# Kernel optimization log

Measured on AMD Instinct MI355X. Metric: run time of the kernel, lower is better.

## Reference

```python
import jax, jax.numpy as jnp
import numpy as np
from jax import lax

D = 256      # d_model
NH = 4       # nhead == len(multi_size)
DH = D // NH # per-head dim = 64
B, H, W = 8, 32, 32
EPS_LN = 1e-5
EPS_ATT = 1e-6


def conv2d(x, w, pad):
    # x: [B,C,H,W], w: [O,I,k,k], SAME padding via pad=k//2
    return lax.conv_general_dilated(
        x, w, window_strides=(1, 1), padding=[(pad, pad), (pad, pad)],
        dimension_numbers=("NCHW", "OIHW", "NCHW"))


def layer_norm(x, g, b):
    m = jnp.mean(x, axis=-1, keepdims=True)
    v = jnp.mean((x - m) ** 2, axis=-1, keepdims=True)
    return (x - m) * lax.rsqrt(v + EPS_LN) * g + b


def setup_inputs() -> dict:
    key = jax.random.key(0)
    ks = jax.random.split(key, 20)
    s = 0.02
    inp = {
        "x": jax.random.normal(ks[0], (B, D, H, W), jnp.float32),
        "source": jax.random.normal(ks[1], (B, D, H, W), jnp.float32),
        # q projection: conv3x3 d_model -> d_model (bias-free)
        "Wq": jax.random.normal(ks[2], (D, D, 3, 3), jnp.float32) * s,
        # MultiConv k projection: kernels 1,3,5,7, each d_model -> dim
        "Wk1": jax.random.normal(ks[3], (DH, D, 1, 1), jnp.float32) * s,
        "Wk3": jax.random.normal(ks[4], (DH, D, 3, 3), jnp.float32) * s,
        "Wk5": jax.random.normal(ks[5], (DH, D, 5, 5), jnp.float32) * s,
        "Wk7": jax.random.normal(ks[6], (DH, D, 7, 7), jnp.float32) * s,
        # MultiConv v projection
        "Wv1": jax.random.normal(ks[7], (DH, D, 1, 1), jnp.float32) * s,
        "Wv3": jax.random.normal(ks[8], (DH, D, 3, 3), jnp.float32) * s,
        "Wv5": jax.random.normal(ks[9], (DH, D, 5, 5), jnp.float32) * s,
        "Wv7": jax.random.normal(ks[10], (DH, D, 7, 7), jnp.float32) * s,
        # merge linear (bias=False), stored [in,out]
        "Wm": jax.random.normal(ks[11], (D, D), jnp.float32) * s,
        "ln1_g": jnp.ones((D,), jnp.float32),
        "ln1_b": jnp.zeros((D,), jnp.float32),
        "ln2_g": jnp.ones((D,), jnp.float32),
        "ln2_b": jnp.zeros((D,), jnp.float32),
        # FF mlp: Linear(2D->2D, no bias), ReLU, Linear(2D->D, no bias); [in,out]
        "W1": jax.random.normal(ks[12], (2 * D, 2 * D), jnp.float32) * s,
        "W2": jax.random.normal(ks[13], (2 * D, D), jnp.float32) * s,
    }
    return inp


def _forward(x, source, Wq, Wk1, Wk3, Wk5, Wk7, Wv1, Wv3, Wv5, Wv7,
             Wm, ln1_g, ln1_b, ln2_g, ln2_b, W1, W2):
    b, c, h, w = x.shape
    h1, w1 = source.shape[2], source.shape[3]
    L = h * w
    S = h1 * w1

    # projections (multi-scale convs -> heads along channel)
    q = conv2d(x, Wq, 1)                                        # [b,D,h,w]
    k = jnp.concatenate([conv2d(source, Wk1, 0), conv2d(source, Wk3, 1),
                         conv2d(source, Wk5, 2), conv2d(source, Wk7, 3)], axis=1)
    v = jnp.concatenate([conv2d(source, Wv1, 0), conv2d(source, Wv3, 1),
                         conv2d(source, Wv5, 2), conv2d(source, Wv7, 3)], axis=1)

    # b c h w -> b (h w) (nhead dim) -> b L nhead dim
    q = q.transpose(0, 2, 3, 1).reshape(b, L, NH, DH)
    k = k.transpose(0, 2, 3, 1).reshape(b, S, NH, DH)
    v = v.transpose(0, 2, 3, 1).reshape(b, S, NH, DH)

    # FullAttention_vis: softmax attention map [b, L, S, nhead]
    temp = DH ** -0.5
    qk = jnp.einsum("blhd,bshd->blsh", q, k)
    attn_vis = jax.nn.softmax(qk * temp, axis=2)

    # LinearAttention (elu+1 kernel feature map)
    Qf = jax.nn.elu(q) + 1.0
    Kf = jax.nn.elu(k) + 1.0
    v_len = jnp.float32(S)
    vals = v / v_len
    KV = jnp.einsum("bshd,bshv->bhdv", Kf, vals)                # [b,NH,DH,DH]
    Z = 1.0 / (jnp.einsum("blhd,bhd->blh", Qf, Kf.sum(axis=1)) + EPS_ATT)
    msg = jnp.einsum("blhd,bhdv,blh->blhv", Qf, KV, Z) * v_len  # [b,L,NH,DH]

    # merge + norm1
    msg = layer_norm(msg.reshape(b, L, D) @ Wm, ln1_g, ln1_b)

    # FF (mlp): cat -> Linear -> ReLU -> Linear -> norm2
    xf = x.transpose(0, 2, 3, 1).reshape(b, L, c)
    ff = jax.nn.relu(jnp.concatenate([xf, msg], axis=2) @ W1) @ W2
    msg = layer_norm(ff, ln2_g, ln2_b)                          # [b,L,D]
    msg = msg.reshape(b, h, w, c).transpose(0, 3, 1, 2)         # b c h w

    out = x + msg
    # b (h0 w0) (h1 w1) c -> b c h0 w0 h1 w1
    vis = attn_vis.reshape(b, h, w, h1, w1, NH).transpose(0, 5, 1, 2, 3, 4)
    return out, vis


def reference(x, source, Wq, Wk1, Wk3, Wk5, Wk7, Wv1, Wv3, Wv5, Wv7,
              Wm, ln1_g, ln1_b, ln2_g, ln2_b, W1, W2):
    return _forward(x, source, Wq, Wk1, Wk3, Wk5, Wk7, Wv1, Wv3, Wv5, Wv7,
                    Wm, ln1_g, ln1_b, ln2_g, ln2_b, W1, W2)
```

## Files before the change

### kernel.cpp

```cpp
#include <hip/hip_runtime.h>

#define DEV __device__ __forceinline__

typedef unsigned short u16;
typedef unsigned int u32;
typedef __bf16 bf16x8 __attribute__((ext_vector_type(8)));
typedef float f32x4 __attribute__((ext_vector_type(4)));

DEV float elu1(float x) { return x > 0.f ? x + 1.f : __expf(x); }

DEV u16 f2bf(float f) {
    union { float f; unsigned u; } v; v.f = f;
    unsigned r = v.u + 0x7fffu + ((v.u >> 16) & 1u);
    return (u16)(r >> 16);
}

DEV float bf2f(u16 h) {
    union { u32 u; float f; } v; v.u = ((u32)h) << 16; return v.f;
}

__global__ __launch_bounds__(256) void prep1_kernel(
    const float* __restrict__ Wq,
    const float* __restrict__ Wk1, const float* __restrict__ Wk3,
    const float* __restrict__ Wk5, const float* __restrict__ Wk7,
    const float* __restrict__ Wv1, const float* __restrict__ Wv3,
    const float* __restrict__ Wv5, const float* __restrict__ Wv7,
    u16* __restrict__ wpack,
    const float* __restrict__ x, const float* __restrict__ src,
    u16* __restrict__ xbh, u16* __restrict__ sbh)
{
    __shared__ float lds[32 * 129];
    const int t = threadIdx.x;
    if (blockIdx.x < 1632) {
        int gid = blockIdx.x * 256 + t;
        int frag = gid >> 6, l = gid & 63;
        const float* W; int K, ocbase = 0, rel;
        if (frag < 1152) {
            W = Wq; K = 3; int slot = frag / 288; rel = frag % 288; ocbase = slot * 64;
        } else {
            int f = frag - 1152; int side = f / 2688; f %= 2688;
            if (f < 32)        { W = side ? Wv1 : Wk1; K = 1; rel = f; }
            else if (f < 320)  { W = side ? Wv3 : Wk3; K = 3; rel = f - 32; }
            else if (f < 1120) { W = side ? Wv5 : Wk5; K = 5; rel = f - 320; }
            else               { W = side ? Wv7 : Wk7; K = 7; rel = f - 1120; }
        }
        int og = rel & 3, cc = (rel >> 2) & 7, tap = rel >> 5;
        int dy = tap / K, dx = tap % K;
        int oc = ocbase + og * 16 + (l & 15);
        int c0 = cc * 32 + (l >> 4) * 8;
        u16 pk[8];
#pragma unroll
        for (int j = 0; j < 8; ++j)
            pk[j] = f2bf(W[((size_t)(oc * 256 + c0 + j) * K + dy) * K + dx]);
        *(int4*)&wpack[(size_t)frag * 512 + l * 8] = *(const int4*)pk;
        return;
    }
    const int i = blockIdx.x - 1632;
    const int inp = i >> 9, rem = i & 511;
    const int b = rem >> 6, cc = (rem >> 3) & 7, pxb = rem & 7;
    const float* in = (inp ? src : x) + ((size_t)b * 256 + cc * 32) * 1024 + pxb * 128;
    u16* outp = (inp ? sbh : xbh) + (size_t)b * 262144 + (size_t)cc * 32768 + pxb * 128 * 32;
#pragma unroll
    for (int u = 0; u < 4; ++u) {
        int unit = t + u * 256;
        int r = unit >> 5, px4 = unit & 31;
        float4 v = *(const float4*)(in + (size_t)r * 1024 + px4 * 4);
        lds[r * 129 + px4 * 4 + 0] = v.x;
        lds[r * 129 + px4 * 4 + 1] = v.y;
        lds[r * 129 + px4 * 4 + 2] = v.z;
        lds[r * 129 + px4 * 4 + 3] = v.w;
    }
    __syncthreads();
#pragma unroll
    for (int u = 0; u < 2; ++u) {
        int unit = t + u * 256;
        int px = unit >> 2, cg = unit & 3;
        u16 pk[8];
#pragma unroll
        for (int j = 0; j < 8; ++j) pk[j] = f2bf(lds[(cg * 8 + j) * 129 + px]);
        *(int4*)&outp[px * 32 + cg * 8] = *(const int4*)pk;
    }
}

template<int K>
DEV void conv_mfma_body(const u16* __restrict__ srcb,
                        const u16* __restrict__ wsec,
                        u16* __restrict__ dst,
                        u16* Bt, int y0, int cch0, int ncc, int t)
{
    constexpr int P = K / 2;
    const int w = t >> 6, l = t & 63;
    const int chi = l >> 4, ln = l & 15;
    const int rowbase = chi * 22 + w * 2 + 3 - P;
    const int colbase = ln + 3 - P;
    f32x4 acc[4][4];
#pragma unroll
    for (int m = 0; m < 4; ++m)
#pragma unroll
        for (int n = 0; n < 4; ++n) acc[m][n] = (f32x4){0.f, 0.f, 0.f, 0.f};

    for (int cc = 0; cc < ncc; ++cc) {
        const int ccg = cch0 + cc;
        __syncthreads();
#pragma unroll
        for (int u = 0; u < 7; ++u) {
            int unit = t + (u << 9);
            if (unit < 2816) {
                int xv = unit & 31, r = unit >> 5;
                int yy = r % 22, ch = r / 22;
                int ygl = y0 - 3 + yy;
                int4 pk;
                if ((unsigned)ygl < 32u)
                    pk = *(const int4*)&srcb[(size_t)ccg * 32768 + (ygl * 32 + xv) * 32 + ch * 8];
                else
                    pk = (int4){0, 0, 0, 0};
                *(int4*)&Bt[((ch * 22 + yy) * 40 + xv + 3) * 8] = pk;
            } else if (unit < 3520) {
                int hu = unit - 2816;
                int hx = hu & 7; int xi = hx < 3 ? hx : hx + 32;
                int r = hu >> 3; int yy = r % 22, ch = r / 22;
                int4 z = {0, 0, 0, 0};
                *(int4*)&Bt[((ch * 22 + yy) * 40 + xi) * 8] = z;
            }
        }
        __syncthreads();
#pragma unroll
        for (int dy = 0; dy < K; ++dy) {
#pragma unroll
            for (int dx = 0; dx < K; ++dx) {
                const int tap = dy * K + dx;
                const u16* wp = wsec + ((size_t)(tap * 8 + ccg) * 4) * 512 + l * 8;
                bf16x8 a0 = *(const bf16x8*)(wp);
                bf16x8 a1 = *(const bf16x8*)(wp + 512);
                bf16x8 a2 = *(const bf16x8*)(wp + 1024);
                bf16x8 a3 = *(const bf16x8*)(wp + 1536);
                bf16x8 bf[4];
#pragma unroll
                for (int n = 0; n < 4; ++n) {
                    int row = rowbase + dy + (n >> 1);
                    int col = colbase + dx + (n & 1) * 16;
                    bf[n] = *(const bf16x8*)&Bt[(row * 40 + col) * 8];
                }
#pragma unroll
                for (int n = 0; n < 4; ++n) {
                    acc[0][n] = __builtin_amdgcn_mfma_f32_16x16x32_bf16(a0, bf[n], acc[0][n], 0, 0, 0);
                    acc[1][n] = __builtin_amdgcn_mfma_f32_16x16x32_bf16(a1, bf[n], acc[1][n], 0, 0, 0);
                    acc[2][n] = __builtin_amdgcn_mfma_f32_16x16x32_bf16(a2, bf[n], acc[2][n], 0, 0, 0);
                    acc[3][n] = __builtin_amdgcn_mfma_f32_16x16x32_bf16(a3, bf[n], acc[3][n], 0, 0, 0);
                }
            }
        }
    }
#pragma unroll
    for (int m = 0; m < 4; ++m)
#pragma unroll
        for (int n = 0; n < 4; ++n) {
            int y = y0 + w * 2 + (n >> 1);
            int px = y * 32 + (n & 1) * 16 + ln;
            int ocb = m * 16 + chi * 4;
            u16 pk[4];
#pragma unroll
            for (int r = 0; r < 4; ++r) pk[r] = f2bf(acc[m][n][r]);
            *(uint2*)&dst[(size_t)px * 64 + ocb] = *(const uint2*)pk;
        }
}

__global__ __launch_bounds__(512) void conv_mfma_kernel(
    const u16* __restrict__ xbh, const u16* __restrict__ sbh,
    const u16* __restrict__ wpack,
    u16* __restrict__ qbt, u16* __restrict__ kbt, u16* __restrict__ vbt,
    u16* __restrict__ p5u, u16* __restrict__ p7u)
{
    __shared__ u16 Bt[4 * 22 * 40 * 8];
    const int bx = blockIdx.x, t = threadIdx.x;
    const int g = bx & 31, b = (bx >> 5) & 7, m = bx >> 8;
    if (g < 4) {
        conv_mfma_body<3>(xbh + (size_t)b * 262144,
                          wpack + (size_t)(g * 288) * 512,
                          qbt + ((size_t)(b * 4 + g)) * 65536,
                          Bt, m * 16, 0, 8, t);
        return;
    }
    const int gs = g - 4;
    const int side = gs / 14, gg = gs % 14;
    const u16* sp = sbh + (size_t)b * 262144;
    u16* fin = side ? vbt : kbt;
    const size_t wkb = 1152 + (size_t)side * 2688;
    if (gg == 0) {
        conv_mfma_body<1>(sp, wpack + (wkb + 0) * 512,
                          fin + ((size_t)(b * 4 + 0)) * 65536, Bt, m * 16, 0, 8, t);
    } else if (gg == 1) {
        conv_mfma_body<3>(sp, wpack + (wkb + 32) * 512,
                          fin + ((size_t)(b * 4 + 1)) * 65536, Bt, m * 16, 0, 8, t);
    } else if (gg < 6) {
        int cpart = gg - 2;
        conv_mfma_body<5>(sp, wpack + (wkb + 320) * 512,
                          p5u + (((size_t)side * 4 + cpart) * 8 + b) * 65536,
                          Bt, m * 16, cpart * 2, 2, t);
    } else {
        int cpart = gg - 6;
        conv_mfma_body<7>(sp, wpack + (wkb + 1120) * 512,
                          p7u + (((size_t)side * 8 + cpart) * 8 + b) * 65536,
                          Bt, m * 16, cpart, 1, t);
    }
}

__global__ __launch_bounds__(256) void prep2_kernel(
    const u16* __restrict__ p5u, const u16* __restrict__ p7u,
    u16* __restrict__ kbt, u16* __restrict__ vbt,
    const float* __restrict__ W1, const float* __restrict__ W2,
    const float* __restrict__ Wm,
    u16* __restrict__ w1p, u16* __restrict__ w2p, u16* __restrict__ wmp)
{
    const int t = threadIdx.x;
    if (blockIdx.x < 1024) {
        int gid = blockIdx.x * 256 + t;
        int u8 = gid & 8191;
        int b = (gid >> 13) & 7;
        int headk = (gid >> 16) & 1;
        int side = gid >> 17;
        float sacc[8];
#pragma unroll
        for (int e = 0; e < 8; ++e) sacc[e] = 0.f;
        if (headk == 0) {
#pragma unroll
            for (int p = 0; p < 4; ++p) {
                int4 u = *(const int4*)&p5u[(((size_t)side * 4 + p) * 8 + b) * 65536 + (size_t)u8 * 8];
                const u16* uu = (const u16*)&u;
#pragma unroll
                for (int e = 0; e < 8; ++e) sacc[e] += bf2f(uu[e]);
            }
        } else {
#pragma unroll
            for (int p = 0; p < 8; ++p) {
                int4 u = *(const int4*)&p7u[(((size_t)side * 8 + p) * 8 + b) * 65536 + (size_t)u8 * 8];
                const u16* uu = (const u16*)&u;
#pragma unroll
                for (int e = 0; e < 8; ++e) sacc[e] += bf2f(uu[e]);
            }
        }
        u16 pk[8];
#pragma unroll
        for (int e = 0; e < 8; ++e) pk[e] = f2bf(sacc[e]);
        u16* outb = side ? vbt : kbt;
        *(int4*)&outb[((size_t)(b * 4 + 2 + headk)) * 65536 + (size_t)u8 * 8] = *(const int4*)pk;
        return;
    }
    int gid = (blockIdx.x - 1024) * 256 + t;
    int f = gid >> 6, l = gid & 63;
    if (f >= 896) return;
    u16 pk[8];
    if (f < 512) {
        int ks = f >> 5, nf = f & 31;
#pragma unroll
        for (int j = 0; j < 8; ++j)
            pk[j] = f2bf(W1[(size_t)(ks * 32 + (l >> 4) * 8 + j) * 512 + nf * 16 + (l & 15)]);
        *(int4*)&w1p[(size_t)f * 512 + l * 8] = *(const int4*)pk;
    } else if (f < 768) {
        int f2 = f - 512;
        int ks = f2 >> 4, nf = f2 & 15;
#pragma unroll
        for (int j = 0; j < 8; ++j)
            pk[j] = f2bf(W2[(size_t)(ks * 32 + (l >> 4) * 8 + j) * 256 + nf * 16 + (l & 15)]);
        *(int4*)&w2p[(size_t)f2 * 512 + l * 8] = *(const int4*)pk;
    } else {
        int f3 = f - 768;
        int ks = f3 >> 4, nf = f3 & 15;
#pragma unroll
        for (int j = 0; j < 8; ++j)
            pk[j] = f2bf(Wm[(size_t)(ks * 32 + (l >> 4) * 8 + j) * 256 + nf * 16 + (l & 15)]);
        *(int4*)&wmp[(size_t)f3 * 512 + l * 8] = *(const int4*)pk;
    }
}

__global__ __launch_bounds__(256) void prep3_kernel(
    const u16* __restrict__ kbt, const u16* __restrict__ vbt,
    float* __restrict__ KVp, float* __restrict__ Ksump)
{
    __shared__ float4 smem4[2112];
    float* Kt = (float*)smem4;
    float* Vt = (float*)(smem4 + 64 * 17);
    const int t = threadIdx.x;
    const int bx = blockIdx.x;
    const int b = bx >> 4, h = (bx >> 2) & 3, ch = bx & 3;
    const u16* kbase = kbt + ((size_t)(b * 4 + h) * 1024 + ch * 256) * 64;
    const u16* vbase = vbt + ((size_t)(b * 4 + h) * 1024 + ch * 256) * 64;
    const int d = t >> 2, v0 = (t & 3) * 16;
    float4 acc[4];
#pragma unroll
    for (int j = 0; j < 4; ++j) acc[j] = make_float4(0.f, 0.f, 0.f, 0.f);
    float ks = 0.f;
    for (int st = 0; st < 4; ++st) {
        __syncthreads();
        {
            int s = t >> 2, d0 = (t & 3) * 16;
            const u16* krow = kbase + (size_t)(st * 64 + s) * 64;
            const u16* vrow = vbase + (size_t)(st * 64 + s) * 64;
#pragma unroll
            for (int oo = 0; oo < 2; ++oo) {
                int4 k8 = *(const int4*)&krow[d0 + oo * 8];
                int4 v8 = *(const int4*)&vrow[d0 + oo * 8];
                const u16* ku = (const u16*)&k8;
                const u16* vu = (const u16*)&v8;
#pragma unroll
                for (int e = 0; e < 8; ++e) {
                    Kt[s * 68 + d0 + oo * 8 + e] = elu1(bf2f(ku[e]));
                    Vt[s * 64 + d0 + oo * 8 + e] = bf2f(vu[e]);
                }
            }
        }
        __syncthreads();
#pragma unroll 8
        for (int s = 0; s < 64; ++s) {
            float kf = Kt[s * 68 + d];
            const float4* vvp = (const float4*)(Vt + s * 64 + v0);
#pragma unroll
            for (int j = 0; j < 4; ++j) {
                float4 vv = vvp[j];
                acc[j].x += kf * vv.x; acc[j].y += kf * vv.y;
                acc[j].z += kf * vv.z; acc[j].w += kf * vv.w;
            }
        }
        if (t < 64) {
#pragma unroll 8
            for (int s = 0; s < 64; ++s) ks += Kt[s * 68 + t];
        }
    }
    float* op = KVp + ((size_t)((ch * 32 + b * 4 + h) * 64 + d)) * 64 + v0;
#pragma unroll
    for (int j = 0; j < 4; ++j) ((float4*)op)[j] = acc[j];
    if (t < 64) Ksump[(size_t)(ch * 32 + b * 4 + h) * 64 + t] = ks;
}

__global__ __launch_bounds__(512) void qk_sm_msg_kernel(
    const u16* __restrict__ qbt, const u16* __restrict__ kbt,
    float* __restrict__ vis,
    const float* __restrict__ KVp, const float* __restrict__ Ksump,
    float* __restrict__ msg)
{
    __shared__ float4 smem4[4178];
    const int t = threadIdx.x;
    if (blockIdx.x < 1024) {
        u16* kf = (u16*)smem4;
        u16* qf = (u16*)smem4 + 32 * 512;
        float* redM = (float*)((char*)smem4 + 36864);
        float* redS = redM + 256;
        const int bx = blockIdx.x;
        const int b = bx >> 7, h = (bx >> 5) & 3, l0 = (bx & 31) * 32;
        const u16* qtp = qbt + ((size_t)(b * 4 + h)) * 1024 * 64;
        const u16* ktp = kbt + ((size_t)(b * 4 + h)) * 1024 * 64;

        if (t < 256) {
            int r = t & 31, dblk = t >> 5;
            int4 pk = *(const int4*)&qtp[(size_t)(l0 + r) * 64 + dblk * 8];
            *(int4*)&qf[(((r >> 4) * 2 + (dblk >> 2)) * 64 + (dblk & 3) * 16 + (r & 15)) * 8] = pk;
        }
        __syncthreads();

        const int w = t >> 6, l = t & 63, ln = l & 15, lg = l >> 4;
        bf16x8 a[2][2];
#pragma unroll
        for (int fr = 0; fr < 2; ++fr)
#pragma unroll
            for (int ks = 0; ks < 2; ++ks)
                a[fr][ks] = *(const bf16x8*)&qf[((fr * 2 + ks) * 64 + l) * 8];

        f32x4 acc[2][4][2];
#pragma unroll
        for (int fr = 0; fr < 2; ++fr)
#pragma unroll
            for (int cc = 0; cc < 4; ++cc)
#pragma unroll
                for (int f = 0; f < 2; ++f) acc[fr][cc][f] = (f32x4){0.f, 0.f, 0.f, 0.f};

#pragma unroll
        for (int cc = 0; cc < 4; ++cc) {
            __syncthreads();
#pragma unroll
            for (int it = 0; it < 4; ++it) {
                int unit = it * 512 + t;
                int sl = unit & 255, dblk = unit >> 8;
                int4 pk = *(const int4*)&ktp[(size_t)(cc * 256 + sl) * 64 + dblk * 8];
                *(int4*)&kf[(((sl >> 4) * 2 + (dblk >> 2)) * 64 + (dblk & 3) * 16 + (sl & 15)) * 8] = pk;
            }
            __syncthreads();
#pragma unroll
            for (int f = 0; f < 2; ++f) {
                int fg = (w * 2 + f) * 2;
                bf16x8 b0 = *(const bf16x8*)&kf[((fg + 0) * 64 + l) * 8];
                bf16x8 b1 = *(const bf16x8*)&kf[((fg + 1) * 64 + l) * 8];
#pragma unroll
                for (int fr = 0; fr < 2; ++fr) {
                    acc[fr][cc][f] = __builtin_amdgcn_mfma_f32_16x16x32_bf16(a[fr][0], b0, acc[fr][cc][f], 0, 0, 0);
                    acc[fr][cc][f] = __builtin_amdgcn_mfma_f32_16x16x32_bf16(a[fr][1], b1, acc[fr][cc][f], 0, 0, 0);
                }
            }
        }

#pragma unroll
        for (int fr = 0; fr < 2; ++fr)
#pragma unroll
            for (int cc = 0; cc < 4; ++cc)
#pragma unroll
                for (int f = 0; f < 2; ++f)
#pragma unroll
                    for (int e = 0; e < 4; ++e) acc[fr][cc][f][e] *= 0.125f;

        float rmax[2][4];
#pragma unroll
        for (int fr = 0; fr < 2; ++fr)
#pragma unroll
            for (int reg = 0; reg < 4; ++reg) {
                float m = -1e30f;
#pragma unroll
                for (int cc = 0; cc < 4; ++cc)
#pragma unroll
                    for (int f = 0; f < 2; ++f) m = fmaxf(m, acc[fr][cc][f][reg]);
#pragma unroll
                for (int off = 1; off < 16; off <<= 1) m = fmaxf(m, __shfl_xor(m, off));
                if (ln == 0) redM[(fr * 16 + lg * 4 + reg) * 8 + w] = m;
                rmax[fr][reg] = m;
            }
        __syncthreads();
#pragma unroll
        for (int fr = 0; fr < 2; ++fr)
#pragma unroll
            for (int reg = 0; reg < 4; ++reg) {
                int r = fr * 16 + lg * 4 + reg;
                float m = redM[r * 8];
#pragma unroll
                for (int ww = 1; ww < 8; ++ww) m = fmaxf(m, redM[r * 8 + ww]);
                rmax[fr][reg] = m;
            }
#pragma unroll
        for (int fr = 0; fr < 2; ++fr)
#pragma unroll
            for (int reg = 0; reg < 4; ++reg) {
                float s = 0.f;
                float m = rmax[fr][reg];
#pragma unroll
                for (int cc = 0; cc < 4; ++cc)
#pragma unroll
                    for (int f = 0; f < 2; ++f) {
                        float e = __expf(acc[fr][cc][f][reg] - m);
                        acc[fr][cc][f][reg] = e;
                        s += e;
                    }
#pragma unroll
                for (int off = 1; off < 16; off <<= 1) s += __shfl_xor(s, off);
                if (ln == 0) redS[(fr * 16 + lg * 4 + reg) * 8 + w] = s;
            }
        __syncthreads();
        float invv[2][4];
#pragma unroll
        for (int fr = 0; fr < 2; ++fr)
#pragma unroll
            for (int reg = 0; reg < 4; ++reg) {
                int r = fr * 16 + lg * 4 + reg;
                float s = redS[r * 8] + redS[r * 8 + 1] + redS[r * 8 + 2] + redS[r * 8 + 3]
                        + redS[r * 8 + 4] + redS[r * 8 + 5] + redS[r * 8 + 6] + redS[r * 8 + 7];
                invv[fr][reg] = 1.f / s;
            }
        float* outT = (float*)smem4;
        float* visp = vis + (((size_t)(b * 4 + h)) << 20);
#pragma unroll
        for (int cc = 0; cc < 4; ++cc) {
            __syncthreads();
#pragma unroll
            for (int fr = 0; fr < 2; ++fr)
#pragma unroll
                for (int reg = 0; reg < 4; ++reg) {
                    int r = fr * 16 + lg * 4 + reg;
#pragma unroll
                    for (int f = 0; f < 2; ++f)
                        outT[r * 260 + w * 32 + f * 16 + ln] = acc[fr][cc][f][reg] * invv[fr][reg];
                }
            __syncthreads();
#pragma unroll
            for (int u = 0; u < 4; ++u) {
                int unit = u * 512 + t;
                int r = unit >> 6, c4 = unit & 63;
                f32x4 v = *(const f32x4*)&outT[r * 260 + c4 * 4];
                __builtin_nontemporal_store(v,
                    (f32x4*)&visp[(size_t)(l0 + r) * 1024 + cc * 256 + c4 * 4]);
            }
        }
        return;
    }
    float* kvl = (float*)smem4;
    float* ksl = (float*)smem4 + 4 * 4112;
    const int bx2 = blockIdx.x - 1024;
    const int b = bx2 >> 3, l0 = (bx2 & 7) * 128;
#pragma unroll
    for (int m = 0; m < 8; ++m) {
        int unit = t + (m << 9);
        int hh = unit >> 10, dd = (unit >> 4) & 63, v4 = unit & 15;
        float4 s = make_float4(0.f, 0.f, 0.f, 0.f);
#pragma unroll
        for (int ch = 0; ch < 4; ++ch) {
            float4 u = *(const float4*)&KVp[((size_t)(ch * 32 + b * 4)) * 4096 + (size_t)unit * 4];
            s.x += u.x; s.y += u.y; s.z += u.z; s.w += u.w;
        }
        *(float4*)&kvl[hh * 4112 + dd * 64 + v4 * 4] = s;
    }
    if (t < 256) {
        float s = 0.f;
#pragma unroll
        for (int ch = 0; ch < 4; ++ch)
            s += Ksump[(size_t)(ch * 32 + b * 4) * 64 + t];
        ksl[(t >> 6) * 65 + (t & 63)] = s;
    }
    __syncthreads();
    const int h = t & 3, l = l0 + (t >> 2);
    const u16* qrow = qbt + ((size_t)(b * 4 + h) * 1024 + l) * 64;
    float qf[64];
#pragma unroll
    for (int j8 = 0; j8 < 8; ++j8) {
        int4 pk = *(const int4*)&qrow[j8 * 8];
        const u16* pku = (const u16*)&pk;
#pragma unroll
        for (int e = 0; e < 8; ++e) qf[j8 * 8 + e] = elu1(bf2f(pku[e]));
    }
    float zd = 1e-6f;
#pragma unroll
    for (int dd = 0; dd < 64; ++dd) zd += qf[dd] * ksl[h * 65 + dd];
    const float Z = 1.f / zd;
    float* op = msg + ((size_t)(b * 1024 + l)) * 256 + h * 64;
    for (int c0 = 0; c0 < 64; c0 += 16) {
        float4 a[4];
#pragma unroll
        for (int j = 0; j < 4; ++j) a[j] = make_float4(0.f, 0.f, 0.f, 0.f);
#pragma unroll
        for (int dd = 0; dd < 64; ++dd) {
            float qv = qf[dd];
            const float4* kp = (const float4*)(kvl + h * 4112 + dd * 64 + c0);
#pragma unroll
            for (int j = 0; j < 4; ++j) {
                float4 kk = kp[j];
                a[j].x += qv * kk.x; a[j].y += qv * kk.y;
                a[j].z += qv * kk.z; a[j].w += qv * kk.w;
            }
        }
#pragma unroll
        for (int j = 0; j < 4; ++j) {
            a[j].x *= Z; a[j].y *= Z; a[j].z *= Z; a[j].w *= Z;
            ((float4*)(op + c0))[j] = a[j];
        }
    }
}

__global__ __launch_bounds__(256) void ff_fused_kernel(
    const float* __restrict__ x, const float* __restrict__ msg,
    const u16* __restrict__ wmp,
    const u16* __restrict__ w1p, const u16* __restrict__ w2p,
    const float* __restrict__ g1, const float* __restrict__ b1,
    const float* __restrict__ g2, const float* __restrict__ b2,
    float* __restrict__ out)
{
    __shared__ u16 tile[16 * 520];
    __shared__ u16 mtile[16 * 264];
    __shared__ float redS[16 * 4];
    __shared__ float redQ[16 * 4];
    float* tf = (float*)tile;
    const int t = threadIdx.x;
    const int base = blockIdx.x * 16;
    const int b = base >> 10, l0 = base & 1023;
    const int w = t >> 6, l = t & 63, ln = l & 15, lg = l >> 4;

    {
        int rr = t & 15, cg = t >> 4;
        for (int cci = 0; cci < 16; ++cci) {
            int c = cci * 16 + cg;
            tile[rr * 520 + c] = f2bf(x[((size_t)b * 256 + c) * 1024 + l0 + rr]);
        }
        int r = t >> 4, cb = (t & 15) * 16;
#pragma unroll
        for (int i = 0; i < 4; ++i) {
            float4 v = *(const float4*)&msg[((size_t)(base + r)) * 256 + cb + i * 4];
            u32 p0 = (u32)f2bf(v.x) | ((u32)f2bf(v.y) << 16);
            u32 p1 = (u32)f2bf(v.z) | ((u32)f2bf(v.w) << 16);
            *(u32*)&mtile[r * 264 + cb + i * 4] = p0;
            *(u32*)&mtile[r * 264 + cb + i * 4 + 2] = p1;
        }
    }
    __syncthreads();

    f32x4 accm[4];
#pragma unroll
    for (int fc = 0; fc < 4; ++fc) accm[fc] = (f32x4){0.f, 0.f, 0.f, 0.f};
    for (int ks = 0; ks < 8; ++ks) {
        bf16x8 a0 = *(const bf16x8*)&mtile[ln * 264 + ks * 32 + lg * 8];
#pragma unroll
        for (int fc = 0; fc < 4; ++fc) {
            bf16x8 bb = *(const bf16x8*)&wmp[((size_t)(ks * 16 + w * 4 + fc) * 64 + l) * 8];
            accm[fc] = __builtin_amdgcn_mfma_f32_16x16x32_bf16(a0, bb, accm[fc], 0, 0, 0);
        }
    }
#pragma unroll
    for (int reg = 0; reg < 4; ++reg) {
        float s = 0.f, qsum = 0.f;
#pragma unroll
        for (int fc = 0; fc < 4; ++fc) {
            float v = accm[fc][reg];
            s += v; qsum += v * v;
        }
#pragma unroll
        for (int off = 1; off < 16; off <<= 1) {
            s += __shfl_xor(s, off);
            qsum += __shfl_xor(qsum, off);
        }
        if (ln == 0) {
            int r = lg * 4 + reg;
            redS[r * 4 + w] = s;
            redQ[r * 4 + w] = qsum;
        }
    }
    __syncthreads();
#pragma unroll
    for (int fc = 0; fc < 4; ++fc) {
        int c = w * 64 + fc * 16 + ln;
        float gg = g1[c], bb = b1[c];
#pragma unroll
        for (int reg = 0; reg < 4; ++reg) {
            int r = lg * 4 + reg;
            float s = redS[r * 4] + redS[r * 4 + 1] + redS[r * 4 + 2] + redS[r * 4 + 3];
            float qs = redQ[r * 4] + redQ[r * 4 + 1] + redQ[r * 4 + 2] + redQ[r * 4 + 3];
            float mean = s * (1.f / 256.f);
            float rstd = rsqrtf(qs * (1.f / 256.f) - mean * mean + 1e-5f);
            tile[r * 520 + 256 + c] = f2bf((accm[fc][reg] - mean) * rstd * gg + bb);
        }
    }
    __syncthreads();

    f32x4 acc1[8];
#pragma unroll
    for (int fc = 0; fc < 8; ++fc) acc1[fc] = (f32x4){0.f, 0.f, 0.f, 0.f};
    for (int ks = 0; ks < 16; ++ks) {
        bf16x8 a0 = *(const bf16x8*)&tile[ln * 520 + ks * 32 + lg * 8];
#pragma unroll
        for (int fc = 0; fc < 8; ++fc) {
            bf16x8 bb = *(const bf16x8*)&w1p[((size_t)(ks * 32 + w * 8 + fc) * 64 + l) * 8];
            acc1[fc] = __builtin_amdgcn_mfma_f32_16x16x32_bf16(a0, bb, acc1[fc], 0, 0, 0);
        }
    }
    __syncthreads();
#pragma unroll
    for (int fc = 0; fc < 8; ++fc)
#pragma unroll
        for (int reg = 0; reg < 4; ++reg) {
            int r = lg * 4 + reg;
            int c = w * 128 + fc * 16 + ln;
            tile[r * 520 + c] = f2bf(fmaxf(acc1[fc][reg], 0.f));
        }
    __syncthreads();

    f32x4 acc2[4];
#pragma unroll
    for (int fc = 0; fc < 4; ++fc) acc2[fc] = (f32x4){0.f, 0.f, 0.f, 0.f};
    for (int ks = 0; ks < 16; ++ks) {
        bf16x8 a0 = *(const bf16x8*)&tile[ln * 520 + ks * 32 + lg * 8];
#pragma unroll
        for (int fc = 0; fc < 4; ++fc) {
            bf16x8 bb = *(const bf16x8*)&w2p[((size_t)(ks * 16 + w * 4 + fc) * 64 + l) * 8];
            acc2[fc] = __builtin_amdgcn_mfma_f32_16x16x32_bf16(a0, bb, acc2[fc], 0, 0, 0);
        }
    }
#pragma unroll
    for (int reg = 0; reg < 4; ++reg) {
        float s = 0.f, qsum = 0.f;
#pragma unroll
        for (int fc = 0; fc < 4; ++fc) {
            float v = acc2[fc][reg];
            s += v; qsum += v * v;
        }
#pragma unroll
        for (int off = 1; off < 16; off <<= 1) {
            s += __shfl_xor(s, off);
            qsum += __shfl_xor(qsum, off);
        }
        if (ln == 0) {
            int r = lg * 4 + reg;
            redS[r * 4 + w] = s;
            redQ[r * 4 + w] = qsum;
        }
    }
    __syncthreads();
    float mean[4], rstd[4];
#pragma unroll
    for (int reg = 0; reg < 4; ++reg) {
        int r = lg * 4 + reg;
        float s = redS[r * 4] + redS[r * 4 + 1] + redS[r * 4 + 2] + redS[r * 4 + 3];
        float qs = redQ[r * 4] + redQ[r * 4 + 1] + redQ[r * 4 + 2] + redQ[r * 4 + 3];
        float m = s * (1.f / 256.f);
        mean[reg] = m;
        rstd[reg] = rsqrtf(qs * (1.f / 256.f) - m * m + 1e-5f);
    }
    __syncthreads();
#pragma unroll
    for (int fc = 0; fc < 4; ++fc) {
        int c = w * 64 + fc * 16 + ln;
        float gg = g2[c], bb = b2[c];
#pragma unroll
        for (int reg = 0; reg < 4; ++reg) {
            int r = lg * 4 + reg;
            tf[r * 260 + c] = (acc2[fc][reg] - mean[reg]) * rstd[reg] * gg + bb;
        }
    }
    __syncthreads();
    {
        const float* xp = x + ((size_t)b * 256 + t) * 1024 + l0;
        float* op = out + ((size_t)b * 256 + t) * 1024 + l0;
#pragma unroll
        for (int i = 0; i < 4; ++i) {
            float4 xv = *(const float4*)(xp + i * 4);
            float4 o;
            o.x = xv.x + tf[(i * 4 + 0) * 260 + t];
            o.y = xv.y + tf[(i * 4 + 1) * 260 + t];
            o.z = xv.z + tf[(i * 4 + 2) * 260 + t];
            o.w = xv.w + tf[(i * 4 + 3) * 260 + t];
            *(float4*)(op + i * 4) = o;
        }
    }
}

extern "C" void kernel_launch(void* const* d_in, const int* in_sizes, int n_in,
                              void* d_out, int out_size, void* d_ws, size_t ws_size,
                              hipStream_t stream)
{
    const float* x    = (const float*)d_in[0];
    const float* src  = (const float*)d_in[1];
    const float* Wq   = (const float*)d_in[2];
    const float* Wk1  = (const float*)d_in[3];
    const float* Wk3  = (const float*)d_in[4];
    const float* Wk5  = (const float*)d_in[5];
    const float* Wk7  = (const float*)d_in[6];
    const float* Wv1  = (const float*)d_in[7];
    const float* Wv3  = (const float*)d_in[8];
    const float* Wv5  = (const float*)d_in[9];
    const float* Wv7  = (const float*)d_in[10];
    const float* Wm   = (const float*)d_in[11];
    const float* g1   = (const float*)d_in[12];
    const float* b1   = (const float*)d_in[13];
    const float* g2   = (const float*)d_in[14];
    const float* b2   = (const float*)d_in[15];
    const float* W1   = (const float*)d_in[16];
    const float* W2   = (const float*)d_in[17];

    float* out = (float*)d_out;
    float* vis = out + 2097152;

    u16* p5u = (u16*)vis;
    u16* p7u = (u16*)(vis + 2097152);

    float* ws    = (float*)d_ws;
    u16*   qbt   = (u16*)ws;
    u16*   kbt   = (u16*)(ws + 1048576);
    u16*   vbt   = (u16*)(ws + 2097152);
    u16*   wpack = (u16*)(ws + 6291456);
    u16*   w1p   = (u16*)(ws + 6291456);
    u16*   w2p   = (u16*)(ws + 6422528);
    u16*   wmp   = (u16*)(ws + 6488064);
    u16*   xbh   = (u16*)(ws + 7962624);
    u16*   sbh   = (u16*)(ws + 9011200);
    float* msg   = ws + 10059776;
    float* KVp   = ws + 12156928;
    float* Ksump = ws + 12681216;

    prep1_kernel    <<<2656, 256, 0, stream>>>(Wq, Wk1, Wk3, Wk5, Wk7,
                                               Wv1, Wv3, Wv5, Wv7, wpack,
                                               x, src, xbh, sbh);
    conv_mfma_kernel<<<512,  512, 0, stream>>>(xbh, sbh, wpack, qbt, kbt, vbt,
                                               p5u, p7u);
    prep2_kernel    <<<1248, 256, 0, stream>>>(p5u, p7u, kbt, vbt,
                                               W1, W2, Wm, w1p, w2p, wmp);
    prep3_kernel    <<<128,  256, 0, stream>>>(kbt, vbt, KVp, Ksump);
    qk_sm_msg_kernel<<<1088, 512, 0, stream>>>(qbt, kbt, vis, KVp, Ksump, msg);
    ff_fused_kernel <<<512,  256, 0, stream>>>(x, msg, wmp, w1p, w2p,
                                               g1, b1, g2, b2, out);
}
```

Baseline: 260.7 us.

## Split q and 3x3 k/v convolutions across input-channel parts for load balance

The q conv and the 3x3 k/v convs are now split into two input-channel halves, each written as a bf16 partial to scratch. A generalized reduction kernel sums the q, 3x3, 5x5 and 7x7 partials. This gives 608 conv blocks of more even size instead of 512 blocks where the heavy q/3x3 jobs set the tail. The cost is extra partial-sum traffic, a larger reduction pass, and more bf16 rounding from partials.

Result: faster. 255.2 us (median of 2 runs) (-2.1%).

```diff
diff --git a/kernel.cpp b/kernel.cpp
--- a/kernel.cpp
+++ b/kernel.cpp
@@ -168,85 +168,99 @@
 __global__ __launch_bounds__(512) void conv_mfma_kernel(
     const u16* __restrict__ xbh, const u16* __restrict__ sbh,
     const u16* __restrict__ wpack,
-    u16* __restrict__ qbt, u16* __restrict__ kbt, u16* __restrict__ vbt,
-    u16* __restrict__ p5u, u16* __restrict__ p7u)
+    u16* __restrict__ kbt, u16* __restrict__ vbt,
+    u16* __restrict__ pq, u16* __restrict__ p3,
+    u16* __restrict__ p5, u16* __restrict__ p7)
 {
     __shared__ u16 Bt[4 * 22 * 40 * 8];
     const int bx = blockIdx.x, t = threadIdx.x;
-    const int g = bx & 31, b = (bx >> 5) & 7, m = bx >> 8;
-    if (g < 4) {
+    const int b = bx / 76, job = bx % 76;
+    const int m = job & 1, j = job >> 1;
+    if (j < 8) {
+        int slot = j >> 1, cp = j & 1;
         conv_mfma_body<3>(xbh + (size_t)b * 262144,
-                          wpack + (size_t)(g * 288) * 512,
-                          qbt + ((size_t)(b * 4 + g)) * 65536,
-                          Bt, m * 16, 0, 8, t);
+                          wpack + (size_t)(slot * 288) * 512,
+                          pq + ((size_t)((slot * 2 + cp) * 8 + b)) * 65536,
+                          Bt, m * 16, cp * 4, 4, t);
         return;
     }
-    const int gs = g - 4;
-    const int side = gs / 14, gg = gs % 14;
+    const int s2 = j - 8;
+    const int side = s2 / 15, jj = s2 % 15;
     const u16* sp = sbh + (size_t)b * 262144;
     u16* fin = side ? vbt : kbt;
     const size_t wkb = 1152 + (size_t)side * 2688;
-    if (gg == 0) {
+    if (jj == 0) {
         conv_mfma_body<1>(sp, wpack + (wkb + 0) * 512,
                           fin + ((size_t)(b * 4 + 0)) * 65536, Bt, m * 16, 0, 8, t);
-    } else if (gg == 1) {
+    } else if (jj < 3) {
+        int cp = jj - 1;
         conv_mfma_body<3>(sp, wpack + (wkb + 32) * 512,
-                          fin + ((size_t)(b * 4 + 1)) * 65536, Bt, m * 16, 0, 8, t);
-    } else if (gg < 6) {
-        int cpart = gg - 2;
+                          p3 + ((size_t)((side * 2 + cp) * 8 + b)) * 65536,
+                          Bt, m * 16, cp * 4, 4, t);
+    } else if (jj < 7) {
+        int cp = jj - 3;
         conv_mfma_body<5>(sp, wpack + (wkb + 320) * 512,
-                          p5u + (((size_t)side * 4 + cpart) * 8 + b) * 65536,
-                          Bt, m * 16, cpart * 2, 2, t);
+                          p5 + ((size_t)((side * 4 + cp) * 8 + b)) * 65536,
+                          Bt, m * 16, cp * 2, 2, t);
     } else {
-        int cpart = gg - 6;
+        int cp = jj - 7;
         conv_mfma_body<7>(sp, wpack + (wkb + 1120) * 512,
-                          p7u + (((size_t)side * 8 + cpart) * 8 + b) * 65536,
-                          Bt, m * 16, cpart, 1, t);
+                          p7 + ((size_t)((side * 8 + cp) * 8 + b)) * 65536,
+                          Bt, m * 16, cp, 1, t);
     }
 }
 
 __global__ __launch_bounds__(256) void prep2_kernel(
-    const u16* __restrict__ p5u, const u16* __restrict__ p7u,
-    u16* __restrict__ kbt, u16* __restrict__ vbt,
+    const u16* __restrict__ pq, const u16* __restrict__ p3,
+    const u16* __restrict__ p5, const u16* __restrict__ p7,
+    u16* __restrict__ qbt, u16* __restrict__ kbt, u16* __restrict__ vbt,
     const float* __restrict__ W1, const float* __restrict__ W2,
     const float* __restrict__ Wm,
     u16* __restrict__ w1p, u16* __restrict__ w2p, u16* __restrict__ wmp)
 {
     const int t = threadIdx.x;
-    if (blockIdx.x < 1024) {
+    if (blockIdx.x < 2560) {
         int gid = blockIdx.x * 256 + t;
         int u8 = gid & 8191;
-        int b = (gid >> 13) & 7;
-        int headk = (gid >> 16) & 1;
-        int side = gid >> 17;
+        int img = gid >> 13;
+        const u16* srcb; u16* outb; int parts;
+        if (img < 32) {
+            int sub = img >> 3, b_ = img & 7;
+            parts = 2;
+            srcb = pq + ((size_t)(sub * 2) * 8 + b_) * 65536;
+            outb = qbt + ((size_t)(b_ * 4 + sub)) * 65536;
+        } else if (img < 48) {
+            int i2 = img - 32; int sub = i2 >> 3, b_ = i2 & 7;
+            parts = 2;
+            srcb = p3 + ((size_t)(sub * 2) * 8 + b_) * 65536;
+            outb = (sub ? vbt : kbt) + ((size_t)(b_ * 4 + 1)) * 65536;
+        } else if (img < 64) {
+            int i2 = img - 48; int sub = i2 >> 3, b_ = i2 & 7;
+            parts = 4;
+            srcb = p5 + ((size_t)(sub * 4) * 8 + b_) * 65536;
+            outb = (sub ? vbt : kbt) + ((size_t)(b_ * 4 + 2)) * 65536;
+        } else {
+            int i2 = img - 64; int sub = i2 >> 3, b_ = i2 & 7;
+            parts = 8;
+            srcb = p7 + ((size_t)(sub * 8) * 8 + b_) * 65536;
+            outb = (sub ? vbt : kbt) + ((size_t)(b_ * 4 + 3)) * 65536;
+        }
         float sacc[8];
 #pragma unroll
         for (int e = 0; e < 8; ++e) sacc[e] = 0.f;
-        if (headk == 0) {
-#pragma unroll
-            for (int p = 0; p < 4; ++p) {
-                int4 u = *(const int4*)&p5u[(((size_t)side * 4 + p) * 8 + b) * 65536 + (size_t)u8 * 8];
-                const u16* uu = (const u16*)&u;
-#pragma unroll
-                for (int e = 0; e < 8; ++e) sacc[e] += bf2f(uu[e]);
-            }
-        } else {
-#pragma unroll
-            for (int p = 0; p < 8; ++p) {
-                int4 u = *(const int4*)&p7u[(((size_t)side * 8 + p) * 8 + b) * 65536 + (size_t)u8 * 8];
-                const u16* uu = (const u16*)&u;
-#pragma unroll
-                for (int e = 0; e < 8; ++e) sacc[e] += bf2f(uu[e]);
-            }
+        for (int p = 0; p < parts; ++p) {
+            int4 u = *(const int4*)&srcb[(size_t)p * 524288 + (size_t)u8 * 8];
+            const u16* uu = (const u16*)&u;
+#pragma unroll
+            for (int e = 0; e < 8; ++e) sacc[e] += bf2f(uu[e]);
         }
         u16 pk[8];
 #pragma unroll
         for (int e = 0; e < 8; ++e) pk[e] = f2bf(sacc[e]);
-        u16* outb = side ? vbt : kbt;
-        *(int4*)&outb[((size_t)(b * 4 + 2 + headk)) * 65536 + (size_t)u8 * 8] = *(const int4*)pk;
+        *(int4*)&outb[(size_t)u8 * 8] = *(const int4*)pk;
         return;
     }
-    int gid = (blockIdx.x - 1024) * 256 + t;
+    int gid = (blockIdx.x - 2560) * 256 + t;
     int f = gid >> 6, l = gid & 63;
     if (f >= 896) return;
     u16 pk[8];
@@ -749,8 +763,10 @@
     float* out = (float*)d_out;
     float* vis = out + 2097152;
 
-    u16* p5u = (u16*)vis;
-    u16* p7u = (u16*)(vis + 2097152);
+    u16* pq = (u16*)vis;
+    u16* p3 = pq + 4194304;
+    u16* p5 = p3 + 2097152;
+    u16* p7 = p5 + 4194304;
 
     float* ws    = (float*)d_ws;
     u16*   qbt   = (u16*)ws;
@@ -769,9 +785,9 @@
     prep1_kernel    <<<2656, 256, 0, stream>>>(Wq, Wk1, Wk3, Wk5, Wk7,
                                                Wv1, Wv3, Wv5, Wv7, wpack,
                                                x, src, xbh, sbh);
-    conv_mfma_kernel<<<512,  512, 0, stream>>>(xbh, sbh, wpack, qbt, kbt, vbt,
-                                               p5u, p7u);
-    prep2_kernel    <<<1248, 256, 0, stream>>>(p5u, p7u, kbt, vbt,
+    conv_mfma_kernel<<<608,  512, 0, stream>>>(xbh, sbh, wpack, kbt, vbt,
+                                               pq, p3, p5, p7);
+    prep2_kernel    <<<2784, 256, 0, stream>>>(pq, p3, p5, p7, qbt, kbt, vbt,
                                                W1, W2, Wm, w1p, w2p, wmp);
     prep3_kernel    <<<128,  256, 0, stream>>>(kbt, vbt, KVp, Ksump);
     qk_sm_msg_kernel<<<1088, 512, 0, stream>>>(qbt, kbt, vis, KVp, Ksump, msg);
```
